# Kernel tuning notes

Hardware: AMD Instinct MI355X
Metric: run time of the kernel (lower is better)

Reference implementation:

```python
import jax, jax.numpy as jnp
import numpy as np

B, N, C, H = 4, 2048, 768, 8
D = C // H          # head_size = 96
D3 = D // 3         # projected channel dim = 32


def _linear(x, W, b):
    # torch convention: W [out, in]
    return x @ W.T + b


def setup_inputs() -> dict:
    key = jax.random.key(0)
    ks = jax.random.split(key, 11)
    s = 0.02
    return {
        "x":   jax.random.normal(ks[0], (B, N, C), dtype=jnp.float32),
        "Wqk": jax.random.normal(ks[1], (C, C), dtype=jnp.float32) * s,
        "bqk": jax.random.normal(ks[2], (C,), dtype=jnp.float32) * s,
        "Wv":  jax.random.normal(ks[3], (C, C), dtype=jnp.float32) * s,
        "bv":  jax.random.normal(ks[4], (C,), dtype=jnp.float32) * s,
        "Wo":  jax.random.normal(ks[5], (C, C), dtype=jnp.float32) * s,
        "bo":  jax.random.normal(ks[6], (C,), dtype=jnp.float32) * s,
        "We":  jax.random.normal(ks[7], (D3, D), dtype=jnp.float32) * s,
        "be":  jax.random.normal(ks[8], (D3,), dtype=jnp.float32) * s,
        "Wf":  jax.random.normal(ks[9], (D3, D), dtype=jnp.float32) * s,
        "bf":  jax.random.normal(ks[10], (D3,), dtype=jnp.float32) * s,
    }


def reference(x, Wqk, bqk, Wv, bv, Wo, bo, We, be, Wf, bf):
    b, n, c = x.shape
    # q and k come from the SAME qk_linear applied twice -> identical tensors
    qk = _linear(x, Wqk, bqk).reshape(b, n, H, D)   # [B,N,H,D]
    v_ = _linear(x, Wv, bv).reshape(b, n, H, D)     # [B,N,H,D]

    q = k = qk  # [B,N,H,D] (used as bhnd via einsum)

    # Branch 1: standard softmax attention over tokens
    scale = 1.0 / jnp.sqrt(jnp.asarray(D, dtype=x.dtype))
    scores = jnp.einsum('bnhd,bmhd->bhnm', q, k) * scale   # [B,H,N,N]
    attn = jax.nn.softmax(scores, axis=-1)                  # dropout: identity (eval)
    out1 = jnp.einsum('bhnm,bmhd->bnhd', attn, v_).reshape(b, n, C)
    out1 = _linear(out1, Wo, bo)

    # Branch 2: Linformer-style projected channel attention (per token)
    k_proj = _linear(k, We, be)    # [B,N,H,D3]
    v_proj = _linear(v_, Wf, bf)   # [B,N,H,D3]
    # k_proj^T @ q over heads: [B,N,D3,D], softmax over D
    attn_sa = jax.nn.softmax(jnp.einsum('bnhe,bnhd->bned', k_proj, q), axis=-1)
    x_ca = jnp.einsum('bnhe,bned->bnhd', v_proj, attn_sa).reshape(b, n, C)
    x_ca = _linear(x_ca, Wo, bo)

    return 0.5 * (out1 + x_ca)
```

## Files before the change

### kernel.cpp

```cpp
#include <hip/hip_runtime.h>
#include <math.h>

#define BSZ 4
#define NTOK 2048
#define CDIM 768
#define HN 8
#define DH 96
#define DP 32
#define MTOT (BSZ * NTOK)

typedef short bf16x8 __attribute__((ext_vector_type(8)));
typedef float f32x4 __attribute__((ext_vector_type(4)));

__device__ __forceinline__ unsigned short f2bf(float f) {
    union { float f; unsigned u; } v; v.f = f;
    unsigned r = v.u + 0x7FFFu + ((v.u >> 16) & 1u);
    return (unsigned short)(r >> 16);
}
__device__ __forceinline__ unsigned short f2bf_trunc(float f) {
    union { float f; unsigned u; } v; v.f = f;
    return (unsigned short)(v.u >> 16);
}
__device__ __forceinline__ float bf2f(unsigned short h) {
    union { unsigned u; float f; } v; v.u = ((unsigned)h) << 16;
    return v.f;
}

__device__ __forceinline__ void async16(const unsigned short* g, unsigned short* l) {
    __builtin_amdgcn_global_load_lds(
        (const __attribute__((address_space(1))) unsigned int*)g,
        (__attribute__((address_space(3))) unsigned int*)l,
        16, 0, 0);
}

#define TE4 1572864
#define WE4 147456
#define WE24 768

__global__ __launch_bounds__(256) void prep(const float* __restrict__ x,
                                            const float* __restrict__ Wqk,
                                            const float* __restrict__ Wv,
                                            const float* __restrict__ Wo,
                                            const float* __restrict__ We,
                                            const float* __restrict__ Wf,
                                            unsigned short* __restrict__ xhi,
                                            unsigned short* __restrict__ wqv,
                                            unsigned short* __restrict__ woh,
                                            unsigned short* __restrict__ webf,
                                            unsigned short* __restrict__ wfbf)
{
    int i = blockIdx.x * 256 + threadIdx.x;
    const float* src; unsigned short* dst; int j;
    if (i < TE4)                        { j = i;                        src = x;   dst = xhi; }
    else if (i < TE4 + WE4)             { j = i - TE4;                  src = Wqk; dst = wqv; }
    else if (i < TE4 + 2 * WE4)         { j = i - TE4 - WE4;            src = Wv;  dst = wqv + (size_t)CDIM * CDIM; }
    else if (i < TE4 + 3 * WE4)         { j = i - TE4 - 2 * WE4;        src = Wo;  dst = woh; }
    else if (i < TE4 + 3 * WE4 + WE24)  { j = i - TE4 - 3 * WE4;        src = We;  dst = webf; }
    else                                { j = i - TE4 - 3 * WE4 - WE24; src = Wf;  dst = wfbf; }
    float4 f = ((const float4*)src)[j];
    ushort4 u;
    u.x = f2bf(f.x); u.y = f2bf(f.y); u.z = f2bf(f.z); u.w = f2bf(f.w);
    ((ushort4*)dst)[j] = u;
}

__global__ __launch_bounds__(256, 3) void gemm_qv(const unsigned short* __restrict__ Ah,
                                                  const unsigned short* __restrict__ wqv,
                                                  const float* __restrict__ bqk,
                                                  const float* __restrict__ bv,
                                                  unsigned short* __restrict__ qkbf,
                                                  unsigned short* __restrict__ vbf,
                                                  unsigned short* __restrict__ vbft)
{
    const int K = CDIM;
    __shared__ __align__(16) unsigned short As[8 * 512];
    __shared__ __align__(16) unsigned short Bs[8 * 512];

    const int tid  = threadIdx.x;
    const int lane = tid & 63;
    const int w    = tid >> 6;
    const int wy   = w >> 1;
    const int wx   = w & 1;
    const int l15  = lane & 15;
    const int quad = lane >> 4;
    const int n0   = blockIdx.x * 128;
    const int m0   = blockIdx.y * 128;

    const int srow   = lane >> 2;
    const int schunk = (lane & 3) ^ ((lane >> 3) & 3);
    const unsigned short* agp[2];
    const unsigned short* bgp[2];
    #pragma unroll
    for (int t = 0; t < 2; ++t) {
        int g = w * 2 + t;
        agp[t] = Ah  + (size_t)(m0 + g * 16 + srow) * K + schunk * 8;
        bgp[t] = wqv + (size_t)(n0 + g * 16 + srow) * K + schunk * 8;
    }

    const int roff = l15 * 32 + (quad ^ ((l15 >> 1) & 3)) * 8;

    f32x4 acc[4][4];
    #pragma unroll
    for (int rb = 0; rb < 4; ++rb)
        #pragma unroll
        for (int cb = 0; cb < 4; ++cb) acc[rb][cb] = (f32x4)0.0f;

    for (int k0 = 0; k0 < K; k0 += 32) {
        #pragma unroll
        for (int t = 0; t < 2; ++t) {
            async16(agp[t] + k0, &As[(w * 2 + t) * 512]);
            async16(bgp[t] + k0, &Bs[(w * 2 + t) * 512]);
        }
        __syncthreads();

        bf16x8 a[4], bfr[4];
        #pragma unroll
        for (int rb = 0; rb < 4; ++rb)
            a[rb] = *(const bf16x8*)&As[(wy * 4 + rb) * 512 + roff];
        #pragma unroll
        for (int cb = 0; cb < 4; ++cb)
            bfr[cb] = *(const bf16x8*)&Bs[(wx * 4 + cb) * 512 + roff];

        #pragma unroll
        for (int rb = 0; rb < 4; ++rb)
            #pragma unroll
            for (int cb = 0; cb < 4; ++cb)
                acc[rb][cb] = __builtin_amdgcn_mfma_f32_16x16x32_bf16(a[rb], bfr[cb], acc[rb][cb], 0, 0, 0);
        __syncthreads();
    }

    const bool isQ = (n0 < CDIM);
    #pragma unroll
    for (int rb = 0; rb < 4; ++rb)
        #pragma unroll
        for (int cb = 0; cb < 4; ++cb)
            #pragma unroll
            for (int r = 0; r < 4; ++r) {
                int row = m0 + wy * 64 + rb * 16 + quad * 4 + r;
                int colg = n0 + wx * 64 + cb * 16 + l15;
                if (isQ) {
                    float val = acc[rb][cb][r] + bqk[colg];
                    qkbf[(size_t)row * CDIM + colg] = f2bf(val);
                } else {
                    int col = colg - CDIM;
                    float val = acc[rb][cb][r] + bv[col];
                    vbf[(size_t)row * CDIM + col] = f2bf(val);
                    int b = row >> 11, tok = row & 2047;
                    int hh = col / DH, dd = col % DH;
                    vbft[(((size_t)b * HN + hh) * DH + dd) * NTOK + tok] = f2bf(val);
                }
            }
}

__global__ __launch_bounds__(256, 3) void gemm_out(const unsigned short* __restrict__ Ah,
                                                   const unsigned short* __restrict__ Bh,
                                                   const float* __restrict__ bias,
                                                   float* __restrict__ Yf)
{
    const int K = CDIM;
    __shared__ __align__(16) unsigned short As[8 * 512];
    __shared__ __align__(16) unsigned short Bs[8 * 512];

    const int tid  = threadIdx.x;
    const int lane = tid & 63;
    const int w    = tid >> 6;
    const int wy   = w >> 1;
    const int wx   = w & 1;
    const int l15  = lane & 15;
    const int quad = lane >> 4;
    const int n0   = blockIdx.x * 128;
    const int m0   = blockIdx.y * 128;

    const int srow   = lane >> 2;
    const int schunk = (lane & 3) ^ ((lane >> 3) & 3);
    const unsigned short* agp[2];
    const unsigned short* bgp[2];
    #pragma unroll
    for (int t = 0; t < 2; ++t) {
        int g = w * 2 + t;
        agp[t] = Ah + (size_t)(m0 + g * 16 + srow) * K + schunk * 8;
        bgp[t] = Bh + (size_t)(n0 + g * 16 + srow) * K + schunk * 8;
    }
    const int roff = l15 * 32 + (quad ^ ((l15 >> 1) & 3)) * 8;

    f32x4 acc[4][4];
    #pragma unroll
    for (int rb = 0; rb < 4; ++rb)
        #pragma unroll
        for (int cb = 0; cb < 4; ++cb) acc[rb][cb] = (f32x4)0.0f;

    for (int k0 = 0; k0 < K; k0 += 32) {
        #pragma unroll
        for (int t = 0; t < 2; ++t) {
            async16(agp[t] + k0, &As[(w * 2 + t) * 512]);
            async16(bgp[t] + k0, &Bs[(w * 2 + t) * 512]);
        }
        __syncthreads();

        bf16x8 a[4], bfr[4];
        #pragma unroll
        for (int rb = 0; rb < 4; ++rb)
            a[rb] = *(const bf16x8*)&As[(wy * 4 + rb) * 512 + roff];
        #pragma unroll
        for (int cb = 0; cb < 4; ++cb)
            bfr[cb] = *(const bf16x8*)&Bs[(wx * 4 + cb) * 512 + roff];

        #pragma unroll
        for (int rb = 0; rb < 4; ++rb)
            #pragma unroll
            for (int cb = 0; cb < 4; ++cb)
                acc[rb][cb] = __builtin_amdgcn_mfma_f32_16x16x32_bf16(a[rb], bfr[cb], acc[rb][cb], 0, 0, 0);
        __syncthreads();
    }

    #pragma unroll
    for (int rb = 0; rb < 4; ++rb)
        #pragma unroll
        for (int cb = 0; cb < 4; ++cb)
            #pragma unroll
            for (int r = 0; r < 4; ++r) {
                int row = m0 + wy * 64 + rb * 16 + quad * 4 + r;
                int col = n0 + wx * 64 + cb * 16 + l15;
                Yf[(size_t)row * CDIM + col] = 0.5f * acc[rb][cb][r] + bias[col];
            }
}

#define PSTR 104

__global__ __launch_bounds__(256) void proj_gemm(const unsigned short* __restrict__ qkbf,
                                                 const unsigned short* __restrict__ vbf,
                                                 const unsigned short* __restrict__ webf,
                                                 const unsigned short* __restrict__ wfbf,
                                                 const float* __restrict__ be,
                                                 const float* __restrict__ bfv,
                                                 float* __restrict__ kp,
                                                 float* __restrict__ vp)
{
    const unsigned short* Abf = blockIdx.y ? vbf : qkbf;
    const unsigned short* Wbf = blockIdx.y ? wfbf : webf;
    const float* bias         = blockIdx.y ? bfv : be;
    float* Y                  = blockIdx.y ? vp : kp;

    __shared__ __align__(16) unsigned short As[128 * PSTR];
    __shared__ __align__(16) unsigned short Bs[32 * PSTR];

    const int tid  = threadIdx.x;
    const int lane = tid & 63;
    const int w    = tid >> 6;
    const int l15  = lane & 15;
    const int quad = lane >> 4;
    const int m0   = blockIdx.x * 128;

    {
        int r = tid & 127;
        int cb = (tid >> 7) * 12;
        #pragma unroll
        for (int t = 0; t < 12; ++t) {
            int c4 = cb + t;
            if (c4 < 24)
                *(ushort4*)&As[r * PSTR + c4 * 4] =
                    *(const ushort4*)&Abf[(size_t)(m0 + r) * DH + c4 * 4];
        }
    }
    #pragma unroll
    for (int t = 0; t < 3; ++t) {
        int idx = tid + t * 256;
        if (idx < 32 * 24) {
            int r = idx / 24, c4 = idx % 24;
            *(ushort4*)&Bs[r * PSTR + c4 * 4] = *(const ushort4*)&Wbf[r * DH + c4 * 4];
        }
    }
    __syncthreads();

    f32x4 acc[2][2];
    #pragma unroll
    for (int rb = 0; rb < 2; ++rb)
        #pragma unroll
        for (int cb = 0; cb < 2; ++cb) acc[rb][cb] = (f32x4)0.0f;

    #pragma unroll
    for (int kf = 0; kf < 3; ++kf) {
        bf16x8 a0 = *(const bf16x8*)&As[(w * 32 + l15) * PSTR + kf * 32 + quad * 8];
        bf16x8 a1 = *(const bf16x8*)&As[(w * 32 + 16 + l15) * PSTR + kf * 32 + quad * 8];
        bf16x8 b0 = *(const bf16x8*)&Bs[(l15) * PSTR + kf * 32 + quad * 8];
        bf16x8 b1 = *(const bf16x8*)&Bs[(16 + l15) * PSTR + kf * 32 + quad * 8];
        acc[0][0] = __builtin_amdgcn_mfma_f32_16x16x32_bf16(a0, b0, acc[0][0], 0, 0, 0);
        acc[0][1] = __builtin_amdgcn_mfma_f32_16x16x32_bf16(a0, b1, acc[0][1], 0, 0, 0);
        acc[1][0] = __builtin_amdgcn_mfma_f32_16x16x32_bf16(a1, b0, acc[1][0], 0, 0, 0);
        acc[1][1] = __builtin_amdgcn_mfma_f32_16x16x32_bf16(a1, b1, acc[1][1], 0, 0, 0);
    }

    #pragma unroll
    for (int rb = 0; rb < 2; ++rb)
        #pragma unroll
        for (int cb = 0; cb < 2; ++cb)
            #pragma unroll
            for (int r = 0; r < 4; ++r) {
                int row = m0 + w * 32 + rb * 16 + quad * 4 + r;
                int col = cb * 16 + l15;
                Y[(size_t)row * DP + col] = acc[rb][cb][r] + bias[col];
            }
}

#define QT 128
#define KT 32
#define PST 40
#define SCL2 0.14724420f

__global__ __launch_bounds__(256) void attn_mfma(const unsigned short* __restrict__ qk_bf,
                                                 const unsigned short* __restrict__ v_bft,
                                                 unsigned short* __restrict__ chi)
{
    __shared__ __align__(16) unsigned short KfS[2][6 * 512];
    __shared__ __align__(16) unsigned short VfS[2][6 * 512];
    __shared__ __align__(16) unsigned short Ps[QT * PST];

    const int tid  = threadIdx.x;
    const int lane = tid & 63;
    const int w    = tid >> 6;
    const int l15  = lane & 15;
    const int quad = lane >> 4;

    const int bid = blockIdx.x;
    const int bh  = (bid & 7) * 4 + ((bid >> 3) & 3);
    const int qt  = bid >> 5;
    const int b   = bh >> 3;
    const int h   = bh & 7;
    const int q0  = qt * QT;

    const unsigned short* qbase = qk_bf + (size_t)b * NTOK * CDIM + h * DH;
    const unsigned short* vtb   = v_bft + (size_t)(b * HN + h) * DH * NTOK;

    bf16x8 qf[2][3];
    #pragma unroll
    for (int rb = 0; rb < 2; ++rb)
        #pragma unroll
        for (int kf = 0; kf < 3; ++kf)
            qf[rb][kf] = *(const bf16x8*)&qbase[(size_t)(q0 + w * 32 + rb * 16 + l15) * CDIM + kf * 32 + quad * 8];

    const int  kjt   = w;
    const int  vd0   = (w - 2) * 3;
    const unsigned short* kgb = qbase + (size_t)(kjt * 16 + l15) * CDIM + quad * 8;
    const unsigned short* vgb = vtb + quad * 8;

    bf16x8 ones;
    #pragma unroll
    for (int i = 0; i < 8; ++i) ones[i] = (short)0x3F80;

    f32x4 o[2][6], ls[2];
    #pragma unroll
    for (int rb = 0; rb < 2; ++rb) {
        ls[rb] = (f32x4)0.0f;
        #pragma unroll
        for (int db = 0; db < 6; ++db) o[rb][db] = (f32x4)0.0f;
    }

    if (w < 2) {
        #pragma unroll
        for (int kf = 0; kf < 3; ++kf)
            async16(kgb + kf * 32, &KfS[0][(kf * 2 + kjt) * 512]);
    } else {
        #pragma unroll
        for (int t = 0; t < 3; ++t)
            async16(vgb + (size_t)((vd0 + t) * 16 + l15) * NTOK, &VfS[0][(vd0 + t) * 512]);
    }
    __syncthreads();

    int cur = 0;
    for (int k0 = 0; k0 < NTOK; k0 += KT) {
        const int nxt = cur ^ 1;
        if (k0 + KT < NTOK) {
            if (w < 2) {
                #pragma unroll
                for (int kf = 0; kf < 3; ++kf)
                    async16(kgb + (size_t)(k0 + KT) * CDIM + kf * 32, &KfS[nxt][(kf * 2 + kjt) * 512]);
            } else {
                #pragma unroll
                for (int t = 0; t < 3; ++t)
                    async16(vgb + (size_t)((vd0 + t) * 16 + l15) * NTOK + k0 + KT, &VfS[nxt][(vd0 + t) * 512]);
            }
        }

        f32x4 s00 = (f32x4)0.0f, s01 = (f32x4)0.0f, s10 = (f32x4)0.0f, s11 = (f32x4)0.0f;
        #pragma unroll
        for (int kf = 0; kf < 3; ++kf) {
            bf16x8 k0f = *(const bf16x8*)&KfS[cur][(kf * 2 + 0) * 512 + lane * 8];
            bf16x8 k1f = *(const bf16x8*)&KfS[cur][(kf * 2 + 1) * 512 + lane * 8];
            s00 = __builtin_amdgcn_mfma_f32_16x16x32_bf16(qf[0][kf], k0f, s00, 0, 0, 0);
            s01 = __builtin_amdgcn_mfma_f32_16x16x32_bf16(qf[0][kf], k1f, s01, 0, 0, 0);
            s10 = __builtin_amdgcn_mfma_f32_16x16x32_bf16(qf[1][kf], k0f, s10, 0, 0, 0);
            s11 = __builtin_amdgcn_mfma_f32_16x16x32_bf16(qf[1][kf], k1f, s11, 0, 0, 0);
        }

        #pragma unroll
        for (int r = 0; r < 4; ++r) {
            int pr0 = w * 32 + quad * 4 + r;
            Ps[pr0 * PST + l15]      = f2bf_trunc(exp2f(s00[r] * SCL2));
            Ps[pr0 * PST + l15 + 16] = f2bf_trunc(exp2f(s01[r] * SCL2));
            int pr1 = pr0 + 16;
            Ps[pr1 * PST + l15]      = f2bf_trunc(exp2f(s10[r] * SCL2));
            Ps[pr1 * PST + l15 + 16] = f2bf_trunc(exp2f(s11[r] * SCL2));
        }

        bf16x8 pf0 = *(const bf16x8*)&Ps[(w * 32 + l15) * PST + quad * 8];
        bf16x8 pf1 = *(const bf16x8*)&Ps[(w * 32 + 16 + l15) * PST + quad * 8];
        ls[0] = __builtin_amdgcn_mfma_f32_16x16x32_bf16(pf0, ones, ls[0], 0, 0, 0);
        ls[1] = __builtin_amdgcn_mfma_f32_16x16x32_bf16(pf1, ones, ls[1], 0, 0, 0);
        #pragma unroll
        for (int db = 0; db < 6; ++db) {
            bf16x8 vf = *(const bf16x8*)&VfS[cur][db * 512 + lane * 8];
            o[0][db] = __builtin_amdgcn_mfma_f32_16x16x32_bf16(pf0, vf, o[0][db], 0, 0, 0);
            o[1][db] = __builtin_amdgcn_mfma_f32_16x16x32_bf16(pf1, vf, o[1][db], 0, 0, 0);
        }

        __syncthreads();
        cur = nxt;
    }

    #pragma unroll
    for (int rb = 0; rb < 2; ++rb)
        #pragma unroll
        for (int r = 0; r < 4; ++r) {
            float inv = 1.0f / ls[rb][r];
            int row = w * 32 + rb * 16 + quad * 4 + r;
            size_t base = ((size_t)b * NTOK + q0 + row) * CDIM + h * DH;
            #pragma unroll
            for (int db = 0; db < 6; ++db)
                chi[base + db * 16 + l15] = f2bf(o[rb][db][r] * inv);
        }
}

#define SFS 97

__global__ __launch_bounds__(256) void branch2_v2(const unsigned short* __restrict__ qkbf,
                                                  const float* __restrict__ kpG,
                                                  const float* __restrict__ vpG,
                                                  unsigned short* __restrict__ chi)
{
    __shared__ float qrowS[CDIM];
    __shared__ float SfS[DP * SFS];
    __shared__ float kpS[HN * DP];
    __shared__ float vpS[HN * DP];
    __shared__ float ps[DP][8];
    __shared__ float invs[DP];

    const int tid = threadIdx.x;
    const size_t tok = blockIdx.x;

    if (tid < 192) {
        ushort4 u = *(const ushort4*)&qkbf[tok * CDIM + tid * 4];
        float4 f;
        f.x = bf2f(u.x); f.y = bf2f(u.y); f.z = bf2f(u.z); f.w = bf2f(u.w);
        *(float4*)&qrowS[tid * 4] = f;
    } else {
        int t = tid - 192;
        ((float4*)kpS)[t] = ((const float4*)(kpG + tok * (HN * DP)))[t];
        ((float4*)vpS)[t] = ((const float4*)(vpG + tok * (HN * DP)))[t];
    }
    __syncthreads();

    #pragma unroll
    for (int t = 0; t < 12; ++t) {
        int idx = tid + t * 256;
        int e = idx / DH, d = idx % DH;
        float s = 0.0f;
        #pragma unroll
        for (int h = 0; h < HN; ++h) s += kpS[h * DP + e] * qrowS[h * DH + d];
        SfS[e * SFS + d] = exp2f(s * 1.44269504f);
    }
    __syncthreads();

    {
        int e = tid >> 3, g = tid & 7;
        float s = 0.0f;
        #pragma unroll
        for (int j = 0; j < 12; ++j) s += SfS[e * SFS + g * 12 + j];
        ps[e][g] = s;
    }
    __syncthreads();
    if (tid < DP) {
        float s = 0.0f;
        #pragma unroll
        for (int g = 0; g < 8; ++g) s += ps[tid][g];
        invs[tid] = 1.0f / s;
    }
    __syncthreads();
    {
        int h = tid >> 5, e = tid & 31;
        vpS[h * DP + e] *= invs[e];
    }
    __syncthreads();

    #pragma unroll
    for (int t = 0; t < 3; ++t) {
        int c = tid + t * 256;
        int h = c / DH, d = c % DH;
        float s = 0.0f;
        #pragma unroll 8
        for (int e = 0; e < DP; ++e) s += vpS[h * DP + e] * SfS[e * SFS + d];
        size_t idx = tok * CDIM + c;
        chi[idx] = f2bf(bf2f(chi[idx]) + s);
    }
}

extern "C" void kernel_launch(void* const* d_in, const int* in_sizes, int n_in,
                              void* d_out, int out_size, void* d_ws, size_t ws_size,
                              hipStream_t stream)
{
    (void)in_sizes; (void)n_in; (void)out_size; (void)ws_size;
    const float* x   = (const float*)d_in[0];
    const float* Wqk = (const float*)d_in[1];
    const float* bqk = (const float*)d_in[2];
    const float* Wv  = (const float*)d_in[3];
    const float* bv  = (const float*)d_in[4];
    const float* Wo  = (const float*)d_in[5];
    const float* bo  = (const float*)d_in[6];
    const float* We  = (const float*)d_in[7];
    const float* be  = (const float*)d_in[8];
    const float* Wf  = (const float*)d_in[9];
    const float* bfv = (const float*)d_in[10];
    float* out = (float*)d_out;

    const size_t TE  = (size_t)MTOT * CDIM;
    const size_t WE  = (size_t)CDIM * CDIM;
    const size_t WE2 = (size_t)DP * DH;
    const size_t PE  = (size_t)MTOT * HN * DP;

    char* p = (char*)d_ws;
    unsigned short* xhi  = (unsigned short*)p;   p += TE * 2;
    unsigned short* qkbf = (unsigned short*)p;   p += TE * 2;
    unsigned short* vbf  = (unsigned short*)p;   p += TE * 2;
    unsigned short* vbft = (unsigned short*)p;   p += TE * 2;
    unsigned short* chi  = (unsigned short*)p;   p += TE * 2;
    unsigned short* wqv  = (unsigned short*)p;   p += 2 * WE * 2;
    unsigned short* woh  = (unsigned short*)p;   p += WE * 2;
    unsigned short* webf = (unsigned short*)p;   p += WE2 * 2;
    unsigned short* wfbf = (unsigned short*)p;   p += WE2 * 2;
    float* kp            = (float*)p;            p += PE * 4;
    float* vp            = (float*)p;            p += PE * 4;

    const int prep_items = TE4 + 3 * WE4 + 2 * WE24;
    prep<<<dim3((prep_items + 255) / 256), 256, 0, stream>>>(
        x, Wqk, Wv, Wo, We, Wf, xhi, wqv, woh, webf, wfbf);

    gemm_qv<<<dim3(2 * CDIM / 128, MTOT / 128), 256, 0, stream>>>(
        xhi, wqv, bqk, bv, qkbf, vbf, vbft);

    proj_gemm<<<dim3(MTOT * HN / 128, 2), 256, 0, stream>>>(
        qkbf, vbf, webf, wfbf, be, bfv, kp, vp);

    attn_mfma<<<dim3((NTOK / QT) * BSZ * HN), 256, 0, stream>>>(qkbf, vbft, chi);

    branch2_v2<<<dim3(MTOT), 256, 0, stream>>>(qkbf, kp, vp, chi);

    gemm_out<<<dim3(CDIM / 128, MTOT / 128), 256, 0, stream>>>(chi, woh, bo, out);
}
```

Measured before the change: 299.4 us.

## Double attention query tile to 256 rows with four row blocks per wave

Raises the attention query tile from 128 to 256 rows, so each wave now computes 64 query rows (four 16-row MFMA blocks) against every shared K/V tile. Each K/V tile staged in LDS is reused by twice as many queries, which halves global K/V traffic and async-copy work per query. The launch bound is set to one block per CU to allow the larger accumulator and register footprint. The cost is that the grid shrinks to about one block per CU, leaving only four waves per CU to hide latency.

```diff
diff --git a/kernel.cpp b/kernel.cpp
--- a/kernel.cpp
+++ b/kernel.cpp
@@ -301,14 +301,14 @@
             }
 }
 
-#define QT 128
+#define QT 256
 #define KT 32
 #define PST 40
 #define SCL2 0.14724420f
 
-__global__ __launch_bounds__(256) void attn_mfma(const unsigned short* __restrict__ qk_bf,
-                                                 const unsigned short* __restrict__ v_bft,
-                                                 unsigned short* __restrict__ chi)
+__global__ __launch_bounds__(256, 1) void attn_mfma(const unsigned short* __restrict__ qk_bf,
+                                                    const unsigned short* __restrict__ v_bft,
+                                                    unsigned short* __restrict__ chi)
 {
     __shared__ __align__(16) unsigned short KfS[2][6 * 512];
     __shared__ __align__(16) unsigned short VfS[2][6 * 512];
@@ -330,12 +330,12 @@
     const unsigned short* qbase = qk_bf + (size_t)b * NTOK * CDIM + h * DH;
     const unsigned short* vtb   = v_bft + (size_t)(b * HN + h) * DH * NTOK;
 
-    bf16x8 qf[2][3];
-    #pragma unroll
-    for (int rb = 0; rb < 2; ++rb)
+    bf16x8 qf[4][3];
+    #pragma unroll
+    for (int rb = 0; rb < 4; ++rb)
         #pragma unroll
         for (int kf = 0; kf < 3; ++kf)
-            qf[rb][kf] = *(const bf16x8*)&qbase[(size_t)(q0 + w * 32 + rb * 16 + l15) * CDIM + kf * 32 + quad * 8];
+            qf[rb][kf] = *(const bf16x8*)&qbase[(size_t)(q0 + w * 64 + rb * 16 + l15) * CDIM + kf * 32 + quad * 8];
 
     const int  kjt   = w;
     const int  vd0   = (w - 2) * 3;
@@ -346,9 +346,9 @@
     #pragma unroll
     for (int i = 0; i < 8; ++i) ones[i] = (short)0x3F80;
 
-    f32x4 o[2][6], ls[2];
-    #pragma unroll
-    for (int rb = 0; rb < 2; ++rb) {
+    f32x4 o[4][6], ls[4];
+    #pragma unroll
+    for (int rb = 0; rb < 4; ++rb) {
         ls[rb] = (f32x4)0.0f;
         #pragma unroll
         for (int db = 0; db < 6; ++db) o[rb][db] = (f32x4)0.0f;
@@ -380,36 +380,41 @@
             }
         }
 
-        f32x4 s00 = (f32x4)0.0f, s01 = (f32x4)0.0f, s10 = (f32x4)0.0f, s11 = (f32x4)0.0f;
+        f32x4 s0[4], s1[4];
+        #pragma unroll
+        for (int rb = 0; rb < 4; ++rb) { s0[rb] = (f32x4)0.0f; s1[rb] = (f32x4)0.0f; }
         #pragma unroll
         for (int kf = 0; kf < 3; ++kf) {
             bf16x8 k0f = *(const bf16x8*)&KfS[cur][(kf * 2 + 0) * 512 + lane * 8];
             bf16x8 k1f = *(const bf16x8*)&KfS[cur][(kf * 2 + 1) * 512 + lane * 8];
-            s00 = __builtin_amdgcn_mfma_f32_16x16x32_bf16(qf[0][kf], k0f, s00, 0, 0, 0);
-            s01 = __builtin_amdgcn_mfma_f32_16x16x32_bf16(qf[0][kf], k1f, s01, 0, 0, 0);
-            s10 = __builtin_amdgcn_mfma_f32_16x16x32_bf16(qf[1][kf], k0f, s10, 0, 0, 0);
-            s11 = __builtin_amdgcn_mfma_f32_16x16x32_bf16(qf[1][kf], k1f, s11, 0, 0, 0);
-        }
-
-        #pragma unroll
-        for (int r = 0; r < 4; ++r) {
-            int pr0 = w * 32 + quad * 4 + r;
-            Ps[pr0 * PST + l15]      = f2bf_trunc(exp2f(s00[r] * SCL2));
-            Ps[pr0 * PST + l15 + 16] = f2bf_trunc(exp2f(s01[r] * SCL2));
-            int pr1 = pr0 + 16;
-            Ps[pr1 * PST + l15]      = f2bf_trunc(exp2f(s10[r] * SCL2));
-            Ps[pr1 * PST + l15 + 16] = f2bf_trunc(exp2f(s11[r] * SCL2));
-        }
-
-        bf16x8 pf0 = *(const bf16x8*)&Ps[(w * 32 + l15) * PST + quad * 8];
-        bf16x8 pf1 = *(const bf16x8*)&Ps[(w * 32 + 16 + l15) * PST + quad * 8];
-        ls[0] = __builtin_amdgcn_mfma_f32_16x16x32_bf16(pf0, ones, ls[0], 0, 0, 0);
-        ls[1] = __builtin_amdgcn_mfma_f32_16x16x32_bf16(pf1, ones, ls[1], 0, 0, 0);
+            #pragma unroll
+            for (int rb = 0; rb < 4; ++rb) {
+                s0[rb] = __builtin_amdgcn_mfma_f32_16x16x32_bf16(qf[rb][kf], k0f, s0[rb], 0, 0, 0);
+                s1[rb] = __builtin_amdgcn_mfma_f32_16x16x32_bf16(qf[rb][kf], k1f, s1[rb], 0, 0, 0);
+            }
+        }
+
+        #pragma unroll
+        for (int rb = 0; rb < 4; ++rb)
+            #pragma unroll
+            for (int r = 0; r < 4; ++r) {
+                int prow = w * 64 + rb * 16 + quad * 4 + r;
+                Ps[prow * PST + l15]      = f2bf_trunc(exp2f(s0[rb][r] * SCL2));
+                Ps[prow * PST + l15 + 16] = f2bf_trunc(exp2f(s1[rb][r] * SCL2));
+            }
+
+        bf16x8 pf[4];
+        #pragma unroll
+        for (int rb = 0; rb < 4; ++rb) {
+            pf[rb] = *(const bf16x8*)&Ps[(w * 64 + rb * 16 + l15) * PST + quad * 8];
+            ls[rb] = __builtin_amdgcn_mfma_f32_16x16x32_bf16(pf[rb], ones, ls[rb], 0, 0, 0);
+        }
         #pragma unroll
         for (int db = 0; db < 6; ++db) {
             bf16x8 vf = *(const bf16x8*)&VfS[cur][db * 512 + lane * 8];
-            o[0][db] = __builtin_amdgcn_mfma_f32_16x16x32_bf16(pf0, vf, o[0][db], 0, 0, 0);
-            o[1][db] = __builtin_amdgcn_mfma_f32_16x16x32_bf16(pf1, vf, o[1][db], 0, 0, 0);
+            #pragma unroll
+            for (int rb = 0; rb < 4; ++rb)
+                o[rb][db] = __builtin_amdgcn_mfma_f32_16x16x32_bf16(pf[rb], vf, o[rb][db], 0, 0, 0);
         }
 
         __syncthreads();
@@ -417,11 +422,11 @@
     }
 
     #pragma unroll
-    for (int rb = 0; rb < 2; ++rb)
+    for (int rb = 0; rb < 4; ++rb)
         #pragma unroll
         for (int r = 0; r < 4; ++r) {
             float inv = 1.0f / ls[rb][r];
-            int row = w * 32 + rb * 16 + quad * 4 + r;
+            int row = w * 64 + rb * 16 + quad * 4 + r;
             size_t base = ((size_t)b * NTOK + q0 + row) * CDIM + h * DH;
             #pragma unroll
             for (int db = 0; db < 6; ++db)
```

New measurement: 329.4 us. +10.0%, slower.
